# Performance work log

Measured on AMD Instinct MI355X. Metric: run time of the kernel, lower is better.

The kernel has to match this reference:

```python
import jax, jax.numpy as jnp
import numpy as np

N_NODES = 100000
N_EDGES = 1600000
DIM = 128


def setup_inputs() -> dict:
    key = jax.random.key(0)
    k1, k2, k3, k4 = jax.random.split(key, 4)
    x = jax.random.normal(k1, (N_NODES, DIM), dtype=jnp.float32)
    edge_index = jax.random.randint(k2, (2, N_EDGES), 0, N_NODES, dtype=jnp.int64)
    scale = 1.0 / np.sqrt(DIM)
    W1 = jax.random.normal(k3, (DIM, DIM), dtype=jnp.float32) * scale
    W2 = jax.random.normal(k4, (DIM, DIM), dtype=jnp.float32) * scale
    b1 = jnp.zeros((DIM,), dtype=jnp.float32)
    b2 = jnp.zeros((DIM,), dtype=jnp.float32)
    return {"x": x, "edge_index": edge_index, "W1": W1, "b1": b1, "W2": W2, "b2": b2}


def _gcn_conv(x, src, dst, dinv, W, b, n):
    # linear transform first (PyG GCNConv), then normalized scatter-add aggregation
    h = x @ W                                   # [N, out]
    norm = dinv[src] * dinv[dst]                # [E+N]
    msg = h[src] * norm[:, None]                # [E+N, out]
    agg = jax.ops.segment_sum(msg, dst, num_segments=n)
    return agg + b


def reference(x, edge_index, W1, b1, W2, b2):
    n = x.shape[0]
    loops = jnp.arange(n, dtype=edge_index.dtype)
    src = jnp.concatenate([edge_index[0], loops])  # add self-loops
    dst = jnp.concatenate([edge_index[1], loops])
    deg = jax.ops.segment_sum(jnp.ones_like(src, dtype=x.dtype), dst, num_segments=n)
    dinv = jnp.where(deg > 0, jax.lax.rsqrt(deg), 0.0)  # D^{-1/2}
    h = _gcn_conv(x, src, dst, dinv, W1, b1, n)
    h = jax.nn.relu(h)
    out = _gcn_conv(h, src, dst, dinv, W2, b2, n)
    return out
```

## Files before the change

### kernel.cpp

```cpp
#include <hip/hip_runtime.h>
#include <hip/hip_bf16.h>
#include <hip/hip_fp16.h>

#define NN 100000
#define DIM 128
#define NB 391
#define BCAP 5120
#define GTILES ((NN + 63) / 64)
#define STP 130

typedef _Float16 f16x8 __attribute__((ext_vector_type(8)));
typedef float f32x4 __attribute__((ext_vector_type(4)));

__global__ void k_init(const float* __restrict__ W1, const float* __restrict__ W2,
                       int* __restrict__ bcur, _Float16* __restrict__ Wt1,
                       _Float16* __restrict__ Wt2) {
    const int b = blockIdx.x;
    const int t = threadIdx.x;
    if (b < 2) {
        const int i = b * 256 + t;
        if (i <= NB) bcur[i] = 0;
        return;
    }
    const int idx = (b - 2) * 256 + t;
    const int which = idx >> 14;
    const int i = idx & 16383;
    const int n = i >> 7, k = i & 127;
    if (which == 0) Wt1[n * DIM + k] = (_Float16)W1[k * DIM + n];
    else            Wt2[n * DIM + k] = (_Float16)W2[k * DIM + n];
}

__global__ void k_binA_gemm1(const float* __restrict__ inF, const _Float16* __restrict__ Wt,
                             _Float16* __restrict__ outH, const int* __restrict__ src,
                             const int* __restrict__ dst, int* __restrict__ bcur,
                             int* __restrict__ binbuf, int E, int nbin) {
    __shared__ int hist[4][NB];
    __shared__ _Float16 st[64][STP];
    const int t  = threadIdx.x;
    const int wv = t >> 6;

    if ((int)blockIdx.x < nbin) {
        for (int i = t; i < 4 * NB; i += 256) ((int*)hist)[i] = 0;
        __syncthreads();

        const int e0 = blockIdx.x * 4096;
        int mys[16], myd[16];
#pragma unroll
        for (int i = 0; i < 16; ++i) {
            const int e = e0 + i * 256 + t;
            int d = -1, s = 0;
            if (e < E) {
                d = dst[e];
                s = src[e];
                atomicAdd(&hist[wv][d >> 8], 1);
            }
            mys[i] = s;
            myd[i] = d;
        }
        __syncthreads();

        for (int b = t; b < NB; b += 256) {
            const int h0 = hist[0][b], h1 = hist[1][b], h2 = hist[2][b], h3 = hist[3][b];
            const int tot = h0 + h1 + h2 + h3;
            const int base = tot ? atomicAdd(&bcur[b], tot) : 0;
            hist[0][b] = base;
            hist[1][b] = base + h0;
            hist[2][b] = base + h0 + h1;
            hist[3][b] = base + h0 + h1 + h2;
        }
        __syncthreads();

#pragma unroll
        for (int i = 0; i < 16; ++i) {
            const int d = myd[i];
            if (d >= 0) {
                const int b = d >> 8;
                const int p = atomicAdd(&hist[wv][b], 1);
                if (p < BCAP) binbuf[b * BCAP + p] = mys[i] | ((d & 255) << 17);
            }
        }
        return;
    }

    const int tile = blockIdx.x - nbin;
    const int row0 = tile * 64;
    const int l    = t & 63;
    const int l15  = l & 15;
    const int lk8  = (l >> 4) << 3;
    const int colw = wv << 5;

    f16x8 bf[2][4];
#pragma unroll
    for (int ct = 0; ct < 2; ++ct)
#pragma unroll
        for (int kt = 0; kt < 4; ++kt)
            bf[ct][kt] = *(const f16x8*)&Wt[(colw + ct * 16 + l15) * DIM + kt * 32 + lk8];

    f32x4 acc[4][2];
#pragma unroll
    for (int rt = 0; rt < 4; ++rt)
#pragma unroll
        for (int ct = 0; ct < 2; ++ct) acc[rt][ct] = (f32x4){0.f, 0.f, 0.f, 0.f};

#pragma unroll
    for (int rt = 0; rt < 4; ++rt) {
        int row = row0 + rt * 16 + l15;
        row = min(row, NN - 1);
        f16x8 a[4];
#pragma unroll
        for (int kt = 0; kt < 4; ++kt) {
            const int k0 = kt * 32 + lk8;
            const float4 v0 = *(const float4*)&inF[row * DIM + k0];
            const float4 v1 = *(const float4*)&inF[row * DIM + k0 + 4];
            f16x8 v;
            v[0] = (_Float16)v0.x; v[1] = (_Float16)v0.y;
            v[2] = (_Float16)v0.z; v[3] = (_Float16)v0.w;
            v[4] = (_Float16)v1.x; v[5] = (_Float16)v1.y;
            v[6] = (_Float16)v1.z; v[7] = (_Float16)v1.w;
            a[kt] = v;
        }
#pragma unroll
        for (int ct = 0; ct < 2; ++ct)
#pragma unroll
            for (int kt = 0; kt < 4; ++kt)
                acc[rt][ct] = __builtin_amdgcn_mfma_f32_16x16x32_f16(a[kt], bf[ct][kt],
                                                                    acc[rt][ct], 0, 0, 0);
    }

#pragma unroll
    for (int rt = 0; rt < 4; ++rt)
#pragma unroll
        for (int r = 0; r < 4; ++r) {
            const int lr = rt * 16 + ((l >> 4) << 2) + r;
            st[lr][colw + l15]      = (_Float16)acc[rt][0][r];
            st[lr][colw + 16 + l15] = (_Float16)acc[rt][1][r];
        }
    __syncthreads();
#pragma unroll
    for (int i = 0; i < 4; ++i) {
        const int lr  = (wv << 4) + (i << 2) + (l >> 4);
        const int row = row0 + lr;
        if (row < NN) {
            const uint4 v = *(const uint4*)&st[lr][l15 << 3];
            *(uint4*)&outH[row * DIM + (l15 << 3)] = v;
        }
    }
}

__global__ void k_fill(const int* __restrict__ bcur, const int* __restrict__ binbuf,
                       int* __restrict__ gcur, float* __restrict__ dinv,
                       int* __restrict__ rowstart, int* __restrict__ rowend,
                       int* __restrict__ csr) {
    __shared__ int cnt4[4][256];
    __shared__ int sc[256];
    __shared__ int sbase;
    const int b  = blockIdx.x;
    const int t  = threadIdx.x;
    const int wv = t >> 6;

#pragma unroll
    for (int w = 0; w < 4; ++w) cnt4[w][t] = 0;
    __syncthreads();
    const int n_e = min(bcur[b], BCAP);
    const int* p = &binbuf[b * BCAP];
    for (int i = t; i < n_e; i += 256) atomicAdd(&cnt4[wv][p[i] >> 17], 1);
    __syncthreads();
    const int c0 = cnt4[0][t], c1 = cnt4[1][t], c2 = cnt4[2][t], c3 = cnt4[3][t];
    const int c = c0 + c1 + c2 + c3;
    sc[t] = c;
    __syncthreads();
    int acc = c;
    for (int d = 1; d < 256; d <<= 1) {
        const int o = (t >= d) ? sc[t - d] : 0;
        __syncthreads();
        acc += o;
        sc[t] = acc;
        __syncthreads();
    }
    if (t == 0) sbase = atomicAdd(gcur, sc[255]);
    __syncthreads();
    const int ex = acc - c + sbase;

    const int node = b * 256 + t;
    if (node < NN) {
        rowstart[node] = ex;
        rowend[node]   = ex + c;
        dinv[node]     = rsqrtf((float)(c + 1));
    }
    cnt4[0][t] = ex;
    cnt4[1][t] = ex + c0;
    cnt4[2][t] = ex + c0 + c1;
    cnt4[3][t] = ex + c0 + c1 + c2;
    __syncthreads();
    for (int i = t; i < n_e; i += 256) {
        const int v = p[i];
        const int pos = atomicAdd(&cnt4[wv][v >> 17], 1);
        csr[pos] = v & 0x1FFFF;
    }
}

__global__ void k_gather1(const _Float16* __restrict__ hsp, _Float16* __restrict__ aggH,
                          const int* __restrict__ csr, const int* __restrict__ rowstart,
                          const int* __restrict__ rowend, const float* __restrict__ dinv,
                          const float* __restrict__ bias) {
    const __half* __restrict__ hs = (const __half*)hsp;
    const int w = (blockIdx.x * blockDim.x + threadIdx.x) >> 6;
    if (w >= NN) return;
    const int lane = threadIdx.x & 63;
    const int off  = lane << 1;

    const int start = __builtin_amdgcn_readfirstlane(rowstart[w]);
    const int end   = __builtin_amdgcn_readfirstlane(rowend[w]);
    const float dw  = dinv[w];

    float2 a0 = {0.f, 0.f}, a1 = {0.f, 0.f}, a2 = {0.f, 0.f}, a3 = {0.f, 0.f};
    {
        const float2 v = __half22float2(*(const __half2*)&hs[w * DIM + off]);
        a0.x = dw * v.x; a0.y = dw * v.y;
    }

    int j = start;
    for (; j + 7 < end; j += 8) {
        const int s0 = __builtin_amdgcn_readfirstlane(csr[j]);
        const int s1 = __builtin_amdgcn_readfirstlane(csr[j + 1]);
        const int s2 = __builtin_amdgcn_readfirstlane(csr[j + 2]);
        const int s3 = __builtin_amdgcn_readfirstlane(csr[j + 3]);
        const int s4 = __builtin_amdgcn_readfirstlane(csr[j + 4]);
        const int s5 = __builtin_amdgcn_readfirstlane(csr[j + 5]);
        const int s6 = __builtin_amdgcn_readfirstlane(csr[j + 6]);
        const int s7 = __builtin_amdgcn_readfirstlane(csr[j + 7]);
        const float d0 = dinv[s0], d1 = dinv[s1], d2 = dinv[s2], d3 = dinv[s3];
        const float d4 = dinv[s4], d5 = dinv[s5], d6 = dinv[s6], d7 = dinv[s7];
        const float2 v0 = __half22float2(*(const __half2*)&hs[s0 * DIM + off]);
        const float2 v1 = __half22float2(*(const __half2*)&hs[s1 * DIM + off]);
        const float2 v2 = __half22float2(*(const __half2*)&hs[s2 * DIM + off]);
        const float2 v3 = __half22float2(*(const __half2*)&hs[s3 * DIM + off]);
        const float2 v4 = __half22float2(*(const __half2*)&hs[s4 * DIM + off]);
        const float2 v5 = __half22float2(*(const __half2*)&hs[s5 * DIM + off]);
        const float2 v6 = __half22float2(*(const __half2*)&hs[s6 * DIM + off]);
        const float2 v7 = __half22float2(*(const __half2*)&hs[s7 * DIM + off]);
        a0.x = fmaf(d0, v0.x, a0.x); a0.y = fmaf(d0, v0.y, a0.y);
        a1.x = fmaf(d1, v1.x, a1.x); a1.y = fmaf(d1, v1.y, a1.y);
        a2.x = fmaf(d2, v2.x, a2.x); a2.y = fmaf(d2, v2.y, a2.y);
        a3.x = fmaf(d3, v3.x, a3.x); a3.y = fmaf(d3, v3.y, a3.y);
        a0.x = fmaf(d4, v4.x, a0.x); a0.y = fmaf(d4, v4.y, a0.y);
        a1.x = fmaf(d5, v5.x, a1.x); a1.y = fmaf(d5, v5.y, a1.y);
        a2.x = fmaf(d6, v6.x, a2.x); a2.y = fmaf(d6, v6.y, a2.y);
        a3.x = fmaf(d7, v7.x, a3.x); a3.y = fmaf(d7, v7.y, a3.y);
    }
    for (; j < end; ++j) {
        const int s0 = __builtin_amdgcn_readfirstlane(csr[j]);
        const float d0 = dinv[s0];
        const float2 v0 = __half22float2(*(const __half2*)&hs[s0 * DIM + off]);
        a0.x = fmaf(d0, v0.x, a0.x); a0.y = fmaf(d0, v0.y, a0.y);
    }

    const float2 bb = {bias[off], bias[off + 1]};
    float2 r = {a0.x + a1.x + a2.x + a3.x, a0.y + a1.y + a2.y + a3.y};
    r.x = fmaxf(fmaf(dw, r.x, bb.x), 0.f);
    r.y = fmaxf(fmaf(dw, r.y, bb.y), 0.f);
    *(__half2*)&aggH[w * DIM + off] = __floats2half2_rn(r.x, r.y);
}

__global__ void k_gemm2(const _Float16* __restrict__ inH, const _Float16* __restrict__ Wt,
                        const float* __restrict__ dinv, _Float16* __restrict__ outH) {
    __shared__ _Float16 st[64][STP];
    const int t = threadIdx.x;
    const int row0 = blockIdx.x * 64;
    const int wv   = t >> 6;
    const int l    = t & 63;
    const int l15  = l & 15;
    const int lk8  = (l >> 4) << 3;
    const int colw = wv << 5;

    f16x8 bf[2][4];
#pragma unroll
    for (int ct = 0; ct < 2; ++ct)
#pragma unroll
        for (int kt = 0; kt < 4; ++kt)
            bf[ct][kt] = *(const f16x8*)&Wt[(colw + ct * 16 + l15) * DIM + kt * 32 + lk8];

    f32x4 acc[4][2];
#pragma unroll
    for (int rt = 0; rt < 4; ++rt)
#pragma unroll
        for (int ct = 0; ct < 2; ++ct) acc[rt][ct] = (f32x4){0.f, 0.f, 0.f, 0.f};

#pragma unroll
    for (int rt = 0; rt < 4; ++rt) {
        int row = row0 + rt * 16 + l15;
        row = min(row, NN - 1);
        f16x8 a[4];
#pragma unroll
        for (int kt = 0; kt < 4; ++kt)
            a[kt] = *(const f16x8*)&inH[row * DIM + kt * 32 + lk8];
#pragma unroll
        for (int ct = 0; ct < 2; ++ct)
#pragma unroll
            for (int kt = 0; kt < 4; ++kt)
                acc[rt][ct] = __builtin_amdgcn_mfma_f32_16x16x32_f16(a[kt], bf[ct][kt],
                                                                    acc[rt][ct], 0, 0, 0);
    }

#pragma unroll
    for (int rt = 0; rt < 4; ++rt)
#pragma unroll
        for (int r = 0; r < 4; ++r) {
            const int lr = rt * 16 + ((l >> 4) << 2) + r;
            const float d = dinv[min(row0 + lr, NN - 1)];
            st[lr][colw + l15]      = (_Float16)(acc[rt][0][r] * d);
            st[lr][colw + 16 + l15] = (_Float16)(acc[rt][1][r] * d);
        }
    __syncthreads();
#pragma unroll
    for (int i = 0; i < 4; ++i) {
        const int lr  = (wv << 4) + (i << 2) + (l >> 4);
        const int row = row0 + lr;
        if (row < NN) {
            const uint4 v = *(const uint4*)&st[lr][l15 << 3];
            *(uint4*)&outH[row * DIM + (l15 << 3)] = v;
        }
    }
}

__global__ void k_gather2(const _Float16* __restrict__ hsp, float* __restrict__ outF,
                          const int* __restrict__ csr, const int* __restrict__ rowstart,
                          const int* __restrict__ rowend, const float* __restrict__ dinv,
                          const float* __restrict__ bias) {
    const __half* __restrict__ hs = (const __half*)hsp;
    const int w = (blockIdx.x * blockDim.x + threadIdx.x) >> 6;
    if (w >= NN) return;
    const int lane = threadIdx.x & 63;
    const int off  = lane << 1;

    const int start = __builtin_amdgcn_readfirstlane(rowstart[w]);
    const int end   = __builtin_amdgcn_readfirstlane(rowend[w]);

    float2 a0 = __half22float2(*(const __half2*)&hs[w * DIM + off]);
    float2 a1 = {0.f, 0.f}, a2 = {0.f, 0.f}, a3 = {0.f, 0.f};

    int j = start;
    for (; j + 7 < end; j += 8) {
        const int s0 = __builtin_amdgcn_readfirstlane(csr[j]);
        const int s1 = __builtin_amdgcn_readfirstlane(csr[j + 1]);
        const int s2 = __builtin_amdgcn_readfirstlane(csr[j + 2]);
        const int s3 = __builtin_amdgcn_readfirstlane(csr[j + 3]);
        const int s4 = __builtin_amdgcn_readfirstlane(csr[j + 4]);
        const int s5 = __builtin_amdgcn_readfirstlane(csr[j + 5]);
        const int s6 = __builtin_amdgcn_readfirstlane(csr[j + 6]);
        const int s7 = __builtin_amdgcn_readfirstlane(csr[j + 7]);
        const float2 v0 = __half22float2(*(const __half2*)&hs[s0 * DIM + off]);
        const float2 v1 = __half22float2(*(const __half2*)&hs[s1 * DIM + off]);
        const float2 v2 = __half22float2(*(const __half2*)&hs[s2 * DIM + off]);
        const float2 v3 = __half22float2(*(const __half2*)&hs[s3 * DIM + off]);
        const float2 v4 = __half22float2(*(const __half2*)&hs[s4 * DIM + off]);
        const float2 v5 = __half22float2(*(const __half2*)&hs[s5 * DIM + off]);
        const float2 v6 = __half22float2(*(const __half2*)&hs[s6 * DIM + off]);
        const float2 v7 = __half22float2(*(const __half2*)&hs[s7 * DIM + off]);
        a0.x += v0.x; a0.y += v0.y;
        a1.x += v1.x; a1.y += v1.y;
        a2.x += v2.x; a2.y += v2.y;
        a3.x += v3.x; a3.y += v3.y;
        a0.x += v4.x; a0.y += v4.y;
        a1.x += v5.x; a1.y += v5.y;
        a2.x += v6.x; a2.y += v6.y;
        a3.x += v7.x; a3.y += v7.y;
    }
    for (; j < end; ++j) {
        const int s0 = __builtin_amdgcn_readfirstlane(csr[j]);
        const float2 v0 = __half22float2(*(const __half2*)&hs[s0 * DIM + off]);
        a0.x += v0.x; a0.y += v0.y;
    }

    const float d = dinv[w];
    const float2 bb = {bias[off], bias[off + 1]};
    float2 r = {a0.x + a1.x + a2.x + a3.x, a0.y + a1.y + a2.y + a3.y};
    float2 o;
    o.x = fmaf(d, r.x, bb.x);
    o.y = fmaf(d, r.y, bb.y);
    *(float2*)&outF[w * DIM + off] = o;
}

extern "C" void kernel_launch(void* const* d_in, const int* in_sizes, int n_in,
                              void* d_out, int out_size, void* d_ws, size_t ws_size,
                              hipStream_t stream) {
    const float* x  = (const float*)d_in[0];
    const int*   ei = (const int*)d_in[1];
    const float* W1 = (const float*)d_in[2];
    const float* b1 = (const float*)d_in[3];
    const float* W2 = (const float*)d_in[4];
    const float* b2 = (const float*)d_in[5];
    float* out = (float*)d_out;

    const int E = in_sizes[1] / 2;
    const int* src = ei;
    const int* dst = ei + E;

    char* ws = (char*)d_ws;
    float*    dinv     = (float*)(ws);
    int*      rowstart = (int*)  (ws + (1 << 20));
    int*      rowend   = (int*)  (ws + (1 << 20) + 524288);
    int*      bcur     = (int*)  (ws + (2 << 20));
    _Float16* Wt1      = (_Float16*)(ws + (2 << 20) + 65536);
    _Float16* Wt2      = (_Float16*)(ws + (2 << 20) + 131072);
    int*      csr      = (int*)  (ws + (4  << 20));
    int*      binbuf   = (int*)  (ws + (11 << 20));
    _Float16* hs       = (_Float16*)(ws + (20 << 20));
    _Float16* aggH     = (_Float16*)(ws + (47 << 20));
    _Float16* hs2      = (_Float16*)(ws + (74 << 20));
    int*      gcur     = bcur + NB;

    const int ABLK = (E + 4095) / 4096;

    k_init<<<130, 256, 0, stream>>>(W1, W2, bcur, Wt1, Wt2);

    k_binA_gemm1<<<ABLK + GTILES, 256, 0, stream>>>(x, Wt1, hs, src, dst, bcur,
                                                    binbuf, E, ABLK);

    k_fill<<<NB, 256, 0, stream>>>(bcur, binbuf, gcur, dinv, rowstart, rowend, csr);

    k_gather1<<<(NN * 64) / 256, 256, 0, stream>>>(hs, aggH, csr, rowstart, rowend,
                                                   dinv, b1);

    k_gemm2<<<GTILES, 256, 0, stream>>>(aggH, Wt2, dinv, hs2);
    k_gather2<<<(NN * 64) / 256, 256, 0, stream>>>(hs2, out, csr, rowstart, rowend,
                                                   dinv, b2);
}
```

Before: 225.8 us.

## Split gather1/gemm2 into halves and overlap gemm2 first half with gather1 second half

Drops the weight-transpose init kernel: bcur is cleared with a memset, and the GEMMs read the fp32 W directly with strided scalar loads, converting to fp16 in registers. Gather1 is split at node 50048. The first half runs alone, then a combined kernel runs gemm2 on the first-half tiles alongside gather1 on the second half, and a final kernel does the remaining gemm2 tiles. The aim is to remove a launch and fill idle compute during the memory-bound gather. In exchange, the uncoalesced strided weight loads are repeated in every GEMM tile and one extra launch is added.

```diff
diff --git a/kernel.cpp b/kernel.cpp
--- a/kernel.cpp
+++ b/kernel.cpp
@@ -8,82 +8,20 @@
 #define BCAP 5120
 #define GTILES ((NN + 63) / 64)
 #define STP 130
+#define H0N 50048
+#define G2T0 782
+#define G2T1 (GTILES - G2T0)
 
 typedef _Float16 f16x8 __attribute__((ext_vector_type(8)));
 typedef float f32x4 __attribute__((ext_vector_type(4)));
 
-__global__ void k_init(const float* __restrict__ W1, const float* __restrict__ W2,
-                       int* __restrict__ bcur, _Float16* __restrict__ Wt1,
-                       _Float16* __restrict__ Wt2) {
-    const int b = blockIdx.x;
-    const int t = threadIdx.x;
-    if (b < 2) {
-        const int i = b * 256 + t;
-        if (i <= NB) bcur[i] = 0;
-        return;
-    }
-    const int idx = (b - 2) * 256 + t;
-    const int which = idx >> 14;
-    const int i = idx & 16383;
-    const int n = i >> 7, k = i & 127;
-    if (which == 0) Wt1[n * DIM + k] = (_Float16)W1[k * DIM + n];
-    else            Wt2[n * DIM + k] = (_Float16)W2[k * DIM + n];
-}
-
-__global__ void k_binA_gemm1(const float* __restrict__ inF, const _Float16* __restrict__ Wt,
-                             _Float16* __restrict__ outH, const int* __restrict__ src,
-                             const int* __restrict__ dst, int* __restrict__ bcur,
-                             int* __restrict__ binbuf, int E, int nbin) {
-    __shared__ int hist[4][NB];
-    __shared__ _Float16 st[64][STP];
-    const int t  = threadIdx.x;
-    const int wv = t >> 6;
-
-    if ((int)blockIdx.x < nbin) {
-        for (int i = t; i < 4 * NB; i += 256) ((int*)hist)[i] = 0;
-        __syncthreads();
-
-        const int e0 = blockIdx.x * 4096;
-        int mys[16], myd[16];
-#pragma unroll
-        for (int i = 0; i < 16; ++i) {
-            const int e = e0 + i * 256 + t;
-            int d = -1, s = 0;
-            if (e < E) {
-                d = dst[e];
-                s = src[e];
-                atomicAdd(&hist[wv][d >> 8], 1);
-            }
-            mys[i] = s;
-            myd[i] = d;
-        }
-        __syncthreads();
-
-        for (int b = t; b < NB; b += 256) {
-            const int h0 = hist[0][b], h1 = hist[1][b], h2 = hist[2][b], h3 = hist[3][b];
-            const int tot = h0 + h1 + h2 + h3;
-            const int base = tot ? atomicAdd(&bcur[b], tot) : 0;
-            hist[0][b] = base;
-            hist[1][b] = base + h0;
-            hist[2][b] = base + h0 + h1;
-            hist[3][b] = base + h0 + h1 + h2;
-        }
-        __syncthreads();
-
-#pragma unroll
-        for (int i = 0; i < 16; ++i) {
-            const int d = myd[i];
-            if (d >= 0) {
-                const int b = d >> 8;
-                const int p = atomicAdd(&hist[wv][b], 1);
-                if (p < BCAP) binbuf[b * BCAP + p] = mys[i] | ((d & 255) << 17);
-            }
-        }
-        return;
-    }
-
-    const int tile = blockIdx.x - nbin;
+
+__device__ __forceinline__ void gemm_f16_body(
+    int tile, int t, const _Float16* __restrict__ inH, const float* __restrict__ W,
+    const float* __restrict__ dinv, _Float16* __restrict__ outH,
+    _Float16 (*st)[STP]) {
     const int row0 = tile * 64;
+    const int wv   = t >> 6;
     const int l    = t & 63;
     const int l15  = l & 15;
     const int lk8  = (l >> 4) << 3;
@@ -93,8 +31,14 @@
 #pragma unroll
     for (int ct = 0; ct < 2; ++ct)
 #pragma unroll
-        for (int kt = 0; kt < 4; ++kt)
-            bf[ct][kt] = *(const f16x8*)&Wt[(colw + ct * 16 + l15) * DIM + kt * 32 + lk8];
+        for (int kt = 0; kt < 4; ++kt) {
+            const int nn = colw + ct * 16 + l15;
+            const int k0 = kt * 32 + lk8;
+            f16x8 v;
+#pragma unroll
+            for (int j = 0; j < 8; ++j) v[j] = (_Float16)W[(k0 + j) * DIM + nn];
+            bf[ct][kt] = v;
+        }
 
     f32x4 acc[4][2];
 #pragma unroll
@@ -108,17 +52,8 @@
         row = min(row, NN - 1);
         f16x8 a[4];
 #pragma unroll
-        for (int kt = 0; kt < 4; ++kt) {
-            const int k0 = kt * 32 + lk8;
-            const float4 v0 = *(const float4*)&inF[row * DIM + k0];
-            const float4 v1 = *(const float4*)&inF[row * DIM + k0 + 4];
-            f16x8 v;
-            v[0] = (_Float16)v0.x; v[1] = (_Float16)v0.y;
-            v[2] = (_Float16)v0.z; v[3] = (_Float16)v0.w;
-            v[4] = (_Float16)v1.x; v[5] = (_Float16)v1.y;
-            v[6] = (_Float16)v1.z; v[7] = (_Float16)v1.w;
-            a[kt] = v;
-        }
+        for (int kt = 0; kt < 4; ++kt)
+            a[kt] = *(const f16x8*)&inH[row * DIM + kt * 32 + lk8];
 #pragma unroll
         for (int ct = 0; ct < 2; ++ct)
 #pragma unroll
@@ -132,8 +67,9 @@
 #pragma unroll
         for (int r = 0; r < 4; ++r) {
             const int lr = rt * 16 + ((l >> 4) << 2) + r;
-            st[lr][colw + l15]      = (_Float16)acc[rt][0][r];
-            st[lr][colw + 16 + l15] = (_Float16)acc[rt][1][r];
+            const float d = dinv[min(row0 + lr, NN - 1)];
+            st[lr][colw + l15]      = (_Float16)(acc[rt][0][r] * d);
+            st[lr][colw + 16 + l15] = (_Float16)(acc[rt][1][r] * d);
         }
     __syncthreads();
 #pragma unroll
@@ -147,67 +83,12 @@
     }
 }
 
-__global__ void k_fill(const int* __restrict__ bcur, const int* __restrict__ binbuf,
-                       int* __restrict__ gcur, float* __restrict__ dinv,
-                       int* __restrict__ rowstart, int* __restrict__ rowend,
-                       int* __restrict__ csr) {
-    __shared__ int cnt4[4][256];
-    __shared__ int sc[256];
-    __shared__ int sbase;
-    const int b  = blockIdx.x;
-    const int t  = threadIdx.x;
-    const int wv = t >> 6;
-
-#pragma unroll
-    for (int w = 0; w < 4; ++w) cnt4[w][t] = 0;
-    __syncthreads();
-    const int n_e = min(bcur[b], BCAP);
-    const int* p = &binbuf[b * BCAP];
-    for (int i = t; i < n_e; i += 256) atomicAdd(&cnt4[wv][p[i] >> 17], 1);
-    __syncthreads();
-    const int c0 = cnt4[0][t], c1 = cnt4[1][t], c2 = cnt4[2][t], c3 = cnt4[3][t];
-    const int c = c0 + c1 + c2 + c3;
-    sc[t] = c;
-    __syncthreads();
-    int acc = c;
-    for (int d = 1; d < 256; d <<= 1) {
-        const int o = (t >= d) ? sc[t - d] : 0;
-        __syncthreads();
-        acc += o;
-        sc[t] = acc;
-        __syncthreads();
-    }
-    if (t == 0) sbase = atomicAdd(gcur, sc[255]);
-    __syncthreads();
-    const int ex = acc - c + sbase;
-
-    const int node = b * 256 + t;
-    if (node < NN) {
-        rowstart[node] = ex;
-        rowend[node]   = ex + c;
-        dinv[node]     = rsqrtf((float)(c + 1));
-    }
-    cnt4[0][t] = ex;
-    cnt4[1][t] = ex + c0;
-    cnt4[2][t] = ex + c0 + c1;
-    cnt4[3][t] = ex + c0 + c1 + c2;
-    __syncthreads();
-    for (int i = t; i < n_e; i += 256) {
-        const int v = p[i];
-        const int pos = atomicAdd(&cnt4[wv][v >> 17], 1);
-        csr[pos] = v & 0x1FFFF;
-    }
-}
-
-__global__ void k_gather1(const _Float16* __restrict__ hsp, _Float16* __restrict__ aggH,
-                          const int* __restrict__ csr, const int* __restrict__ rowstart,
-                          const int* __restrict__ rowend, const float* __restrict__ dinv,
-                          const float* __restrict__ bias) {
-    const __half* __restrict__ hs = (const __half*)hsp;
-    const int w = (blockIdx.x * blockDim.x + threadIdx.x) >> 6;
-    if (w >= NN) return;
-    const int lane = threadIdx.x & 63;
-    const int off  = lane << 1;
+__device__ __forceinline__ void gather1_body(
+    int w, int lane, const __half* __restrict__ hs, _Float16* __restrict__ aggH,
+    const int* __restrict__ csr, const int* __restrict__ rowstart,
+    const int* __restrict__ rowend, const float* __restrict__ dinv,
+    const float* __restrict__ bias) {
+    const int off = lane << 1;
 
     const int start = __builtin_amdgcn_readfirstlane(rowstart[w]);
     const int end   = __builtin_amdgcn_readfirstlane(rowend[w]);
@@ -262,12 +143,61 @@
     *(__half2*)&aggH[w * DIM + off] = __floats2half2_rn(r.x, r.y);
 }
 
-__global__ void k_gemm2(const _Float16* __restrict__ inH, const _Float16* __restrict__ Wt,
-                        const float* __restrict__ dinv, _Float16* __restrict__ outH) {
+
+__global__ void k_binA_gemm1(const float* __restrict__ inF, const float* __restrict__ W,
+                             _Float16* __restrict__ outH, const int* __restrict__ src,
+                             const int* __restrict__ dst, int* __restrict__ bcur,
+                             int* __restrict__ binbuf, int E, int nbin) {
+    __shared__ int hist[4][NB];
     __shared__ _Float16 st[64][STP];
-    const int t = threadIdx.x;
-    const int row0 = blockIdx.x * 64;
-    const int wv   = t >> 6;
+    const int t  = threadIdx.x;
+    const int wv = t >> 6;
+
+    if ((int)blockIdx.x < nbin) {
+        for (int i = t; i < 4 * NB; i += 256) ((int*)hist)[i] = 0;
+        __syncthreads();
+
+        const int e0 = blockIdx.x * 4096;
+        int mys[16], myd[16];
+#pragma unroll
+        for (int i = 0; i < 16; ++i) {
+            const int e = e0 + i * 256 + t;
+            int d = -1, s = 0;
+            if (e < E) {
+                d = dst[e];
+                s = src[e];
+                atomicAdd(&hist[wv][d >> 8], 1);
+            }
+            mys[i] = s;
+            myd[i] = d;
+        }
+        __syncthreads();
+
+        for (int b = t; b < NB; b += 256) {
+            const int h0 = hist[0][b], h1 = hist[1][b], h2 = hist[2][b], h3 = hist[3][b];
+            const int tot = h0 + h1 + h2 + h3;
+            const int base = tot ? atomicAdd(&bcur[b], tot) : 0;
+            hist[0][b] = base;
+            hist[1][b] = base + h0;
+            hist[2][b] = base + h0 + h1;
+            hist[3][b] = base + h0 + h1 + h2;
+        }
+        __syncthreads();
+
+#pragma unroll
+        for (int i = 0; i < 16; ++i) {
+            const int d = myd[i];
+            if (d >= 0) {
+                const int b = d >> 8;
+                const int p = atomicAdd(&hist[wv][b], 1);
+                if (p < BCAP) binbuf[b * BCAP + p] = mys[i] | ((d & 255) << 17);
+            }
+        }
+        return;
+    }
+
+    const int tile = blockIdx.x - nbin;
+    const int row0 = tile * 64;
     const int l    = t & 63;
     const int l15  = l & 15;
     const int lk8  = (l >> 4) << 3;
@@ -277,8 +207,14 @@
 #pragma unroll
     for (int ct = 0; ct < 2; ++ct)
 #pragma unroll
-        for (int kt = 0; kt < 4; ++kt)
-            bf[ct][kt] = *(const f16x8*)&Wt[(colw + ct * 16 + l15) * DIM + kt * 32 + lk8];
+        for (int kt = 0; kt < 4; ++kt) {
+            const int nn = colw + ct * 16 + l15;
+            const int k0 = kt * 32 + lk8;
+            f16x8 v;
+#pragma unroll
+            for (int j = 0; j < 8; ++j) v[j] = (_Float16)W[(k0 + j) * DIM + nn];
+            bf[ct][kt] = v;
+        }
 
     f32x4 acc[4][2];
 #pragma unroll
@@ -292,8 +228,17 @@
         row = min(row, NN - 1);
         f16x8 a[4];
 #pragma unroll
-        for (int kt = 0; kt < 4; ++kt)
-            a[kt] = *(const f16x8*)&inH[row * DIM + kt * 32 + lk8];
+        for (int kt = 0; kt < 4; ++kt) {
+            const int k0 = kt * 32 + lk8;
+            const float4 v0 = *(const float4*)&inF[row * DIM + k0];
+            const float4 v1 = *(const float4*)&inF[row * DIM + k0 + 4];
+            f16x8 v;
+            v[0] = (_Float16)v0.x; v[1] = (_Float16)v0.y;
+            v[2] = (_Float16)v0.z; v[3] = (_Float16)v0.w;
+            v[4] = (_Float16)v1.x; v[5] = (_Float16)v1.y;
+            v[6] = (_Float16)v1.z; v[7] = (_Float16)v1.w;
+            a[kt] = v;
+        }
 #pragma unroll
         for (int ct = 0; ct < 2; ++ct)
 #pragma unroll
@@ -307,9 +252,8 @@
 #pragma unroll
         for (int r = 0; r < 4; ++r) {
             const int lr = rt * 16 + ((l >> 4) << 2) + r;
-            const float d = dinv[min(row0 + lr, NN - 1)];
-            st[lr][colw + l15]      = (_Float16)(acc[rt][0][r] * d);
-            st[lr][colw + 16 + l15] = (_Float16)(acc[rt][1][r] * d);
+            st[lr][colw + l15]      = (_Float16)acc[rt][0][r];
+            st[lr][colw + 16 + l15] = (_Float16)acc[rt][1][r];
         }
     __syncthreads();
 #pragma unroll
@@ -321,6 +265,89 @@
             *(uint4*)&outH[row * DIM + (l15 << 3)] = v;
         }
     }
+}
+
+__global__ void k_fill(const int* __restrict__ bcur, const int* __restrict__ binbuf,
+                       int* __restrict__ gcur, float* __restrict__ dinv,
+                       int* __restrict__ rowstart, int* __restrict__ rowend,
+                       int* __restrict__ csr) {
+    __shared__ int cnt4[4][256];
+    __shared__ int sc[256];
+    __shared__ int sbase;
+    const int b  = blockIdx.x;
+    const int t  = threadIdx.x;
+    const int wv = t >> 6;
+
+#pragma unroll
+    for (int w = 0; w < 4; ++w) cnt4[w][t] = 0;
+    __syncthreads();
+    const int n_e = min(bcur[b], BCAP);
+    const int* p = &binbuf[b * BCAP];
+    for (int i = t; i < n_e; i += 256) atomicAdd(&cnt4[wv][p[i] >> 17], 1);
+    __syncthreads();
+    const int c0 = cnt4[0][t], c1 = cnt4[1][t], c2 = cnt4[2][t], c3 = cnt4[3][t];
+    const int c = c0 + c1 + c2 + c3;
+    sc[t] = c;
+    __syncthreads();
+    int acc = c;
+    for (int d = 1; d < 256; d <<= 1) {
+        const int o = (t >= d) ? sc[t - d] : 0;
+        __syncthreads();
+        acc += o;
+        sc[t] = acc;
+        __syncthreads();
+    }
+    if (t == 0) sbase = atomicAdd(gcur, sc[255]);
+    __syncthreads();
+    const int ex = acc - c + sbase;
+
+    const int node = b * 256 + t;
+    if (node < NN) {
+        rowstart[node] = ex;
+        rowend[node]   = ex + c;
+        dinv[node]     = rsqrtf((float)(c + 1));
+    }
+    cnt4[0][t] = ex;
+    cnt4[1][t] = ex + c0;
+    cnt4[2][t] = ex + c0 + c1;
+    cnt4[3][t] = ex + c0 + c1 + c2;
+    __syncthreads();
+    for (int i = t; i < n_e; i += 256) {
+        const int v = p[i];
+        const int pos = atomicAdd(&cnt4[wv][v >> 17], 1);
+        csr[pos] = v & 0x1FFFF;
+    }
+}
+
+__global__ void k_gather1a(const _Float16* __restrict__ hsp, _Float16* __restrict__ aggH,
+                           const int* __restrict__ csr, const int* __restrict__ rowstart,
+                           const int* __restrict__ rowend, const float* __restrict__ dinv,
+                           const float* __restrict__ bias) {
+    const int w = (blockIdx.x * blockDim.x + threadIdx.x) >> 6;
+    gather1_body(w, threadIdx.x & 63, (const __half*)hsp, aggH, csr, rowstart, rowend,
+                 dinv, bias);
+}
+
+__global__ void k_g1_g2(const _Float16* __restrict__ hsp, _Float16* __restrict__ aggH,
+                        const float* __restrict__ W2, const float* __restrict__ dinv,
+                        _Float16* __restrict__ hs2, const int* __restrict__ csr,
+                        const int* __restrict__ rowstart, const int* __restrict__ rowend,
+                        const float* __restrict__ bias) {
+    __shared__ _Float16 st[64][STP];
+    if ((int)blockIdx.x < G2T0) {
+        gemm_f16_body(blockIdx.x, threadIdx.x, aggH, W2, dinv, hs2, st);
+        return;
+    }
+    const int w = H0N + (((blockIdx.x - G2T0) * blockDim.x + threadIdx.x) >> 6);
+    if (w >= NN) return;
+    gather1_body(w, threadIdx.x & 63, (const __half*)hsp, aggH, csr, rowstart, rowend,
+                 dinv, bias);
+}
+
+__global__ void k_gemm2b(const _Float16* __restrict__ inH, const float* __restrict__ W2,
+                         const float* __restrict__ dinv, _Float16* __restrict__ outH) {
+    __shared__ _Float16 st[64][STP];
+    gemm_f16_body(G2T0 + blockIdx.x, threadIdx.x, inH, W2, dinv, outH, st);
 }
 
 __global__ void k_gather2(const _Float16* __restrict__ hsp, float* __restrict__ outF,
@@ -401,8 +428,6 @@
     int*      rowstart = (int*)  (ws + (1 << 20));
     int*      rowend   = (int*)  (ws + (1 << 20) + 524288);
     int*      bcur     = (int*)  (ws + (2 << 20));
-    _Float16* Wt1      = (_Float16*)(ws + (2 << 20) + 65536);
-    _Float16* Wt2      = (_Float16*)(ws + (2 << 20) + 131072);
     int*      csr      = (int*)  (ws + (4  << 20));
     int*      binbuf   = (int*)  (ws + (11 << 20));
     _Float16* hs       = (_Float16*)(ws + (20 << 20));
@@ -412,17 +437,20 @@
 
     const int ABLK = (E + 4095) / 4096;
 
-    k_init<<<130, 256, 0, stream>>>(W1, W2, bcur, Wt1, Wt2);
-
-    k_binA_gemm1<<<ABLK + GTILES, 256, 0, stream>>>(x, Wt1, hs, src, dst, bcur,
+    hipMemsetAsync(bcur, 0, (NB + 1) * sizeof(int), stream);
+
+    k_binA_gemm1<<<ABLK + GTILES, 256, 0, stream>>>(x, W1, hs, src, dst, bcur,
                                                     binbuf, E, ABLK);
 
     k_fill<<<NB, 256, 0, stream>>>(bcur, binbuf, gcur, dinv, rowstart, rowend, csr);
 
-    k_gather1<<<(NN * 64) / 256, 256, 0, stream>>>(hs, aggH, csr, rowstart, rowend,
-                                                   dinv, b1);
-
-    k_gemm2<<<GTILES, 256, 0, stream>>>(aggH, Wt2, dinv, hs2);
+    k_gather1a<<<H0N / 4, 256, 0, stream>>>(hs, aggH, csr, rowstart, rowend, dinv, b1);
+
+    k_g1_g2<<<G2T0 + (NN - H0N) / 4, 256, 0, stream>>>(hs, aggH, W2, dinv, hs2,
+                                                       csr, rowstart, rowend, b1);
+
+    k_gemm2b<<<G2T1, 256, 0, stream>>>(aggH, W2, dinv, hs2);
+
     k_gather2<<<(NN * 64) / 256, 256, 0, stream>>>(hs2, out, csr, rowstart, rowend,
                                                    dinv, b2);
 }
```

Result: slower. 240.0 us (+6.3%).
